# Performance work log

Measured on AMD Instinct MI355X. Metric: run time of the kernel, lower is better.

Reference implementation:

```python
import jax, jax.numpy as jnp
import numpy as np

N, M, D = 20000, 16000, 128

def setup_inputs() -> dict:
    key = jax.random.key(0)
    ks = jax.random.split(key, 4)
    return {
        "clear_feature": jax.random.normal(ks[0], (N, D), dtype=jnp.float32),
        "rain_feature": jax.random.normal(ks[1], (M, D), dtype=jnp.float32),
        # torch nn.Linear weight layout: (out_features, in_features)
        "W1": jax.random.normal(ks[2], (D, 2 * D), dtype=jnp.float32) * 0.05,
        "b1": jnp.zeros((D,), dtype=jnp.float32),
        "W2": jax.random.normal(ks[3], (1, D), dtype=jnp.float32) * 0.05,
        "b2": jnp.zeros((1,), dtype=jnp.float32),
    }

def reference(clear_feature, rain_feature, W1, b1, W2, b2):
    # --- KNN alignment (k=1): argmin of squared Euclidean distance == cdist+topk(smallest) ---
    x2 = jnp.sum(clear_feature * clear_feature, axis=-1, keepdims=True)   # [N,1]
    y2 = jnp.sum(rain_feature * rain_feature, axis=-1)                    # [M]
    d2 = x2 + y2 - 2.0 * (clear_feature @ rain_feature.T)                 # [N,M]
    idx = jnp.argmin(d2, axis=-1)                                         # [N]
    aligned = rain_feature[idx]                                           # [N,D] gather
    # --- attention MLP: Linear(2D->D) + ReLU + Linear(D->1) + Sigmoid ---
    comb = jnp.concatenate([clear_feature, aligned], axis=-1)             # [N,2D]
    h = jax.nn.relu(comb @ W1.T + b1)                                     # [N,D]
    w = jax.nn.sigmoid(h @ W2.T + b2)                                     # [N,1]
    # --- gated fusion ---
    return w * clear_feature + (1.0 - w) * aligned
```

## Files before the change

kernel.cpp:

```cpp
#include <hip/hip_runtime.h>
#include <stdint.h>

#define NN 20000
#define MM 16000
#define DD 128
#define NTILES_M 125
#define SPLITS 8
#define NBLK 157

typedef unsigned long long u64;
typedef _Float16 f16x8 __attribute__((ext_vector_type(8)));
typedef float f32x16 __attribute__((ext_vector_type(16)));

__global__ void k_init_keys(u64* keys) {
    int i = blockIdx.x * 256 + threadIdx.x;
    if (i < NN) keys[i] = ~0ull;
}

__global__ void k_y2(const float* __restrict__ rain, float* __restrict__ y2) {
    int row = blockIdx.x * 4 + (threadIdx.x >> 6);
    int lane = threadIdx.x & 63;
    if (row >= MM) return;
    float2 v = ((const float2*)(rain + (size_t)row * DD))[lane];
    float s = v.x * v.x + v.y * v.y;
    #pragma unroll
    for (int off = 32; off > 0; off >>= 1) s += __shfl_down(s, off);
    if (lane == 0) y2[row] = s;
}

__global__ void k_split_A(const float* __restrict__ clear_f,
                          _Float16* __restrict__ Ahi, _Float16* __restrict__ Alo) {
    int id = blockIdx.x * 256 + threadIdx.x;
    if (id >= NN * 16) return;
    int row = id >> 4, kc = id & 15;
    const float4* src = (const float4*)(clear_f + (size_t)row * DD + kc * 8);
    float4 v0 = src[0], v1 = src[1];
    float x[8] = {v0.x, v0.y, v0.z, v0.w, v1.x, v1.y, v1.z, v1.w};
    _Float16 hi[8], lo[8];
    #pragma unroll
    for (int j = 0; j < 8; ++j) {
        float s = -2.f * x[j];
        _Float16 h = (_Float16)s;
        hi[j] = h;
        lo[j] = (_Float16)(s - (float)h);
    }
    *(f16x8*)(Ahi + (size_t)row * DD + (size_t)kc * 8) = *(f16x8*)hi;
    *(f16x8*)(Alo + (size_t)row * DD + (size_t)kc * 8) = *(f16x8*)lo;
}

__global__ void k_split_B(const float* __restrict__ rain, _Float16* __restrict__ Bimg) {
    int id = blockIdx.x * 256 + threadIdx.x;
    if (id >= MM * 16) return;
    int row = id >> 4, kp = id & 15;
    int tile = row >> 7, c = row & 127;
    int cg = c >> 5, cc = c & 31;
    int kstep = kp >> 1, kh = kp & 1;
    int chunk = ((kstep * 4 + cg) * 2 + kh) * 32 + cc;
    const float4* src = (const float4*)(rain + (size_t)row * DD + kp * 8);
    float4 v0 = src[0], v1 = src[1];
    float x[8] = {v0.x, v0.y, v0.z, v0.w, v1.x, v1.y, v1.z, v1.w};
    _Float16 hi[8], lo[8];
    #pragma unroll
    for (int j = 0; j < 8; ++j) {
        _Float16 h = (_Float16)x[j];
        hi[j] = h;
        lo[j] = (_Float16)(x[j] - (float)h);
    }
    size_t tbase = (size_t)tile * 32768;
    *(f16x8*)(Bimg + tbase + (size_t)chunk * 8) = *(f16x8*)hi;
    *(f16x8*)(Bimg + tbase + 16384 + (size_t)chunk * 8) = *(f16x8*)lo;
}

__global__ __launch_bounds__(256, 2) void k_dist(
        const _Float16* __restrict__ Ahi, const _Float16* __restrict__ Alo,
        const _Float16* __restrict__ Bimg, const float* __restrict__ y2,
        u64* __restrict__ keys) {
    __shared__ _Float16 lds[32768];

    const int tid = threadIdx.x;
    const int w = tid >> 6, lane = tid & 63;
    const int l5 = lane >> 5, l31 = lane & 31;
    const int id = blockIdx.x;
    const int split = id & 7;
    const int n0 = (id >> 3) * 128;

    int arow = n0 + w * 32 + l31;
    if (arow >= NN) arow = NN - 1;
    const _Float16* ap = Ahi + (size_t)arow * DD + l5 * 8;
    const _Float16* lp = Alo + (size_t)arow * DD + l5 * 8;
    f16x8 afh[8], afl[8];
    #pragma unroll
    for (int ks = 0; ks < 8; ++ks) {
        afh[ks] = *(const f16x8*)(ap + ks * 16);
        afl[ks] = *(const f16x8*)(lp + ks * 16);
    }

    float bestd[16];
    int bestcol[16];
    #pragma unroll
    for (int r = 0; r < 16; ++r) { bestd[r] = 1e30f; bestcol[r] = 0; }

    for (int t = split; t < NTILES_M; t += SPLITS) {
        float y2v[4];
        #pragma unroll
        for (int cg = 0; cg < 4; ++cg) y2v[cg] = y2[t * 128 + cg * 32 + l31];

        {
            const _Float16* gsrc = Bimg + (size_t)t * 32768;
            #pragma unroll
            for (int n = 0; n < 16; ++n) {
                int seg = w * 16 + n;
                const _Float16* gp = gsrc + (size_t)seg * 512 + (size_t)lane * 8;
                _Float16* dst = lds + (size_t)seg * 512;
                __builtin_amdgcn_global_load_lds(
                    (const __attribute__((address_space(1))) unsigned int*)gp,
                    (__attribute__((address_space(3))) unsigned int*)dst,
                    16, 0, 0);
            }
        }
        __syncthreads();

        f32x16 acc[4];
        #pragma unroll
        for (int cg = 0; cg < 4; ++cg)
            #pragma unroll
            for (int e = 0; e < 16; ++e) acc[cg][e] = 0.f;

        #pragma unroll
        for (int ks = 0; ks < 8; ++ks) {
            f16x8 bh[4], bl[4];
            #pragma unroll
            for (int cg = 0; cg < 4; ++cg) {
                int chunk = (ks * 4 + cg) * 64 + lane;
                bh[cg] = *(const f16x8*)(lds + (size_t)chunk * 8);
                bl[cg] = *(const f16x8*)(lds + 16384 + (size_t)chunk * 8);
            }
            #pragma unroll
            for (int cg = 0; cg < 4; ++cg) {
                acc[cg] = __builtin_amdgcn_mfma_f32_32x32x16_f16(afh[ks], bh[cg], acc[cg], 0, 0, 0);
                acc[cg] = __builtin_amdgcn_mfma_f32_32x32x16_f16(afh[ks], bl[cg], acc[cg], 0, 0, 0);
                acc[cg] = __builtin_amdgcn_mfma_f32_32x32x16_f16(afl[ks], bh[cg], acc[cg], 0, 0, 0);
            }
        }

        int cb0 = t * 128 + l31;
        #pragma unroll
        for (int r = 0; r < 16; ++r) {
            float d0 = acc[0][r] + y2v[0];
            float d1 = acc[1][r] + y2v[1];
            float d2 = acc[2][r] + y2v[2];
            float d3 = acc[3][r] + y2v[3];
            float tmin = fminf(fminf(d0, d1), fminf(d2, d3));
            int nc = (d0 <= tmin) ? cb0
                   : (d1 <= tmin) ? cb0 + 32
                   : (d2 <= tmin) ? cb0 + 64 : cb0 + 96;
            bool upd = tmin < bestd[r];
            bestd[r] = upd ? tmin : bestd[r];
            bestcol[r] = upd ? nc : bestcol[r];
        }
        __syncthreads();
    }

    #pragma unroll
    for (int r = 0; r < 16; ++r) {
        unsigned u = __float_as_uint(bestd[r]);
        u ^= (unsigned)((int)u >> 31) | 0x80000000u;
        u64 key = ((u64)u << 32) | (unsigned)bestcol[r];
        #pragma unroll
        for (int off = 1; off < 32; off <<= 1) {
            u64 o = __shfl_xor(key, off);
            if (o < key) key = o;
        }
        if (l31 == 0) {
            int grow = n0 + w * 32 + (r & 3) + 8 * (r >> 2) + 4 * l5;
            if (grow < NN) atomicMin(&keys[grow], key);
        }
    }
}

__global__ __launch_bounds__(256) void k_mlp(const float* __restrict__ clear_f,
                                             const float* __restrict__ rain_f,
                                             const float* __restrict__ W1,
                                             const float* __restrict__ b1,
                                             const float* __restrict__ W2,
                                             const float* __restrict__ b2,
                                             const u64* __restrict__ keys,
                                             float* __restrict__ out) {
    __shared__ float comb_s[16][260];
    __shared__ float w1_s[64][132];
    __shared__ float red_s[16][17];
    __shared__ float w_s[16];

    const int tid = threadIdx.x;
    const int n0 = blockIdx.x * 16;

    {
        int r = tid >> 4;
        int t = tid & 15;
        int n = n0 + r;
        unsigned idx = (unsigned)(keys[n] & 0xffffffffu);
        const float4* cp = (const float4*)(clear_f + (size_t)n * DD);
        const float4* rp = (const float4*)(rain_f + (size_t)idx * DD);
        *(float4*)&comb_s[r][4 * t] = cp[t];
        *(float4*)&comb_s[r][4 * (t + 16)] = cp[t + 16];
        *(float4*)&comb_s[r][DD + 4 * t] = rp[t];
        *(float4*)&comb_s[r][DD + 4 * (t + 16)] = rp[t + 16];
    }

    const int r = tid & 15;
    const int g = tid >> 4;
    const int d8 = g * 8;
    float h[8] = {};
    for (int kt = 0; kt < 4; ++kt) {
        __syncthreads();
        #pragma unroll
        for (int i = 0; i < 32; ++i) {
            int lin = i * 256 + tid;
            int d = lin & 127;
            int kk = lin >> 7;
            w1_s[kk][d] = W1[(size_t)d * 256 + kt * 64 + kk];
        }
        __syncthreads();
        #pragma unroll
        for (int kk = 0; kk < 64; ++kk) {
            float c = comb_s[r][kt * 64 + kk];
            float4 wa = *(const float4*)&w1_s[kk][d8];
            float4 wb = *(const float4*)&w1_s[kk][d8 + 4];
            h[0] = fmaf(c, wa.x, h[0]);
            h[1] = fmaf(c, wa.y, h[1]);
            h[2] = fmaf(c, wa.z, h[2]);
            h[3] = fmaf(c, wa.w, h[3]);
            h[4] = fmaf(c, wb.x, h[4]);
            h[5] = fmaf(c, wb.y, h[5]);
            h[6] = fmaf(c, wb.z, h[6]);
            h[7] = fmaf(c, wb.w, h[7]);
        }
    }
    float part = 0.f;
    #pragma unroll
    for (int j = 0; j < 8; ++j) {
        float hv = h[j] + b1[d8 + j];
        hv = hv > 0.f ? hv : 0.f;
        part = fmaf(hv, W2[d8 + j], part);
    }
    red_s[r][g] = part;
    __syncthreads();
    if (tid < 16) {
        float s = 0.f;
        #pragma unroll
        for (int g2 = 0; g2 < 16; ++g2) s += red_s[tid][g2];
        s += b2[0];
        w_s[tid] = 1.f / (1.f + expf(-s));
    }
    __syncthreads();
    {
        int rw = tid >> 4;
        int c8 = (tid & 15) * 8;
        float wv = w_s[rw];
        float ov[8];
        #pragma unroll
        for (int j = 0; j < 8; ++j) {
            float cv = comb_s[rw][c8 + j];
            float av = comb_s[rw][DD + c8 + j];
            ov[j] = wv * cv + (1.f - wv) * av;
        }
        float4* o = (float4*)(out + (size_t)(n0 + rw) * DD + c8);
        o[0] = make_float4(ov[0], ov[1], ov[2], ov[3]);
        o[1] = make_float4(ov[4], ov[5], ov[6], ov[7]);
    }
}

extern "C" void kernel_launch(void* const* d_in, const int* in_sizes, int n_in,
                              void* d_out, int out_size, void* d_ws, size_t ws_size,
                              hipStream_t stream) {
    const float* clear_f = (const float*)d_in[0];
    const float* rain_f = (const float*)d_in[1];
    const float* W1 = (const float*)d_in[2];
    const float* b1 = (const float*)d_in[3];
    const float* W2 = (const float*)d_in[4];
    const float* b2 = (const float*)d_in[5];
    float* out = (float*)d_out;

    char* ws = (char*)d_ws;
    u64* keys = (u64*)ws;
    float* y2 = (float*)(ws + 160000);
    _Float16* Ahi = (_Float16*)(ws + 224000);
    _Float16* Alo = (_Float16*)(ws + 5344000);
    _Float16* Bimg = (_Float16*)(ws + 10464000);

    k_init_keys<<<(NN + 255) / 256, 256, 0, stream>>>(keys);
    k_y2<<<MM / 4, 256, 0, stream>>>(rain_f, y2);
    k_split_A<<<(NN * 16 + 255) / 256, 256, 0, stream>>>(clear_f, Ahi, Alo);
    k_split_B<<<(MM * 16 + 255) / 256, 256, 0, stream>>>(rain_f, Bimg);
    k_dist<<<NBLK * SPLITS, 256, 0, stream>>>(Ahi, Alo, Bimg, y2, keys);
    k_mlp<<<NN / 16, 256, 0, stream>>>(clear_f, rain_f, W1, b1, W2, b2, keys, out);
}
```

Baseline: 418.1 us.

## Retile distance kernel to 256x32 tiles with double-buffered LDS prefetch

The distance kernel now has each wave compute 64 A-rows against 32-column B tiles, so each block covers 256 rows. The next B tile is prefetched into a second LDS buffer while MFMAs run on the current one, and the grid is a 2D layout of 79 row blocks by 13 splits. The B image layout is simplified to match the 32-column tiles. The MLP kernel's W1 load is transposed so global reads are coalesced, with the LDS row padded to 133. Doubling the A fragments in registers raises register pressure and could lower occupancy.

```diff
diff --git a/kernel.cpp b/kernel.cpp
--- a/kernel.cpp
+++ b/kernel.cpp
@@ -4,9 +4,9 @@
 #define NN 20000
 #define MM 16000
 #define DD 128
-#define NTILES_M 125
-#define SPLITS 8
-#define NBLK 157
+#define CT 500
+#define SPLITS 13
+#define RB 79
 
 typedef unsigned long long u64;
 typedef _Float16 f16x8 __attribute__((ext_vector_type(8)));
@@ -51,11 +51,10 @@
 __global__ void k_split_B(const float* __restrict__ rain, _Float16* __restrict__ Bimg) {
     int id = blockIdx.x * 256 + threadIdx.x;
     if (id >= MM * 16) return;
-    int row = id >> 4, kp = id & 15;
-    int tile = row >> 7, c = row & 127;
-    int cg = c >> 5, cc = c & 31;
-    int kstep = kp >> 1, kh = kp & 1;
-    int chunk = ((kstep * 4 + cg) * 2 + kh) * 32 + cc;
+    int cl = id & 31;
+    int kp = (id >> 5) & 15;
+    int tc = id >> 9;
+    int row = tc * 32 + cl;
     const float4* src = (const float4*)(rain + (size_t)row * DD + kp * 8);
     float4 v0 = src[0], v1 = src[1];
     float x[8] = {v0.x, v0.y, v0.z, v0.w, v1.x, v1.y, v1.z, v1.w};
@@ -66,113 +65,131 @@
         hi[j] = h;
         lo[j] = (_Float16)(x[j] - (float)h);
     }
-    size_t tbase = (size_t)tile * 32768;
-    *(f16x8*)(Bimg + tbase + (size_t)chunk * 8) = *(f16x8*)hi;
-    *(f16x8*)(Bimg + tbase + 16384 + (size_t)chunk * 8) = *(f16x8*)lo;
+    size_t base = (size_t)tc * 8192;
+    int chunk = kp * 32 + cl;
+    *(f16x8*)(Bimg + base + (size_t)chunk * 8) = *(f16x8*)hi;
+    *(f16x8*)(Bimg + base + 4096 + (size_t)chunk * 8) = *(f16x8*)lo;
 }
 
 __global__ __launch_bounds__(256, 2) void k_dist(
         const _Float16* __restrict__ Ahi, const _Float16* __restrict__ Alo,
         const _Float16* __restrict__ Bimg, const float* __restrict__ y2,
         u64* __restrict__ keys) {
-    __shared__ _Float16 lds[32768];
+    __shared__ _Float16 lds[2][8192];
 
     const int tid = threadIdx.x;
     const int w = tid >> 6, lane = tid & 63;
     const int l5 = lane >> 5, l31 = lane & 31;
-    const int id = blockIdx.x;
-    const int split = id & 7;
-    const int n0 = (id >> 3) * 128;
-
-    int arow = n0 + w * 32 + l31;
-    if (arow >= NN) arow = NN - 1;
-    const _Float16* ap = Ahi + (size_t)arow * DD + l5 * 8;
-    const _Float16* lp = Alo + (size_t)arow * DD + l5 * 8;
-    f16x8 afh[8], afl[8];
-    #pragma unroll
-    for (int ks = 0; ks < 8; ++ks) {
-        afh[ks] = *(const f16x8*)(ap + ks * 16);
-        afl[ks] = *(const f16x8*)(lp + ks * 16);
-    }
-
-    float bestd[16];
-    int bestcol[16];
-    #pragma unroll
-    for (int r = 0; r < 16; ++r) { bestd[r] = 1e30f; bestcol[r] = 0; }
-
-    for (int t = split; t < NTILES_M; t += SPLITS) {
-        float y2v[4];
-        #pragma unroll
-        for (int cg = 0; cg < 4; ++cg) y2v[cg] = y2[t * 128 + cg * 32 + l31];
-
-        {
-            const _Float16* gsrc = Bimg + (size_t)t * 32768;
+    const int split = blockIdx.y;
+    const int n0 = blockIdx.x * 256;
+
+    f16x8 afh0[8], afl0[8], afh1[8], afl1[8];
+    {
+        int r0 = n0 + w * 64 + l31;       if (r0 >= NN) r0 = NN - 1;
+        int r1 = n0 + w * 64 + 32 + l31;  if (r1 >= NN) r1 = NN - 1;
+        const _Float16* h0 = Ahi + (size_t)r0 * DD + l5 * 8;
+        const _Float16* o0 = Alo + (size_t)r0 * DD + l5 * 8;
+        const _Float16* h1 = Ahi + (size_t)r1 * DD + l5 * 8;
+        const _Float16* o1 = Alo + (size_t)r1 * DD + l5 * 8;
+        #pragma unroll
+        for (int ks = 0; ks < 8; ++ks) {
+            afh0[ks] = *(const f16x8*)(h0 + ks * 16);
+            afl0[ks] = *(const f16x8*)(o0 + ks * 16);
+            afh1[ks] = *(const f16x8*)(h1 + ks * 16);
+            afl1[ks] = *(const f16x8*)(o1 + ks * 16);
+        }
+    }
+
+    float bestd[32];
+    int bestcol[32];
+    #pragma unroll
+    for (int s = 0; s < 32; ++s) { bestd[s] = 1e30f; bestcol[s] = 0; }
+
+    const int nt = (CT - split + SPLITS - 1) / SPLITS;
+
+    {
+        const _Float16* gsrc = Bimg + (size_t)split * 8192;
+        #pragma unroll
+        for (int n = 0; n < 4; ++n) {
+            int seg = w * 4 + n;
+            __builtin_amdgcn_global_load_lds(
+                (const __attribute__((address_space(1))) unsigned int*)
+                    (gsrc + (size_t)seg * 512 + (size_t)lane * 8),
+                (__attribute__((address_space(3))) unsigned int*)
+                    (&lds[0][0] + (size_t)seg * 512),
+                16, 0, 0);
+        }
+    }
+    __syncthreads();
+
+    int p = 0;
+    for (int i = 0; i < nt; ++i) {
+        const int t = split + i * SPLITS;
+
+        if (i + 1 < nt) {
+            const _Float16* gsrc = Bimg + (size_t)(t + SPLITS) * 8192;
+            _Float16* lbase = &lds[1 - p][0];
             #pragma unroll
-            for (int n = 0; n < 16; ++n) {
-                int seg = w * 16 + n;
-                const _Float16* gp = gsrc + (size_t)seg * 512 + (size_t)lane * 8;
-                _Float16* dst = lds + (size_t)seg * 512;
+            for (int n = 0; n < 4; ++n) {
+                int seg = w * 4 + n;
                 __builtin_amdgcn_global_load_lds(
-                    (const __attribute__((address_space(1))) unsigned int*)gp,
-                    (__attribute__((address_space(3))) unsigned int*)dst,
+                    (const __attribute__((address_space(1))) unsigned int*)
+                        (gsrc + (size_t)seg * 512 + (size_t)lane * 8),
+                    (__attribute__((address_space(3))) unsigned int*)
+                        (lbase + (size_t)seg * 512),
                     16, 0, 0);
             }
         }
+
+        float y2v = y2[t * 32 + l31];
+
+        f32x16 acc0, acc1;
+        #pragma unroll
+        for (int e = 0; e < 16; ++e) { acc0[e] = 0.f; acc1[e] = 0.f; }
+
+        const _Float16* lbuf = &lds[p][0];
+        #pragma unroll
+        for (int ks = 0; ks < 8; ++ks) {
+            f16x8 bh = *(const f16x8*)(lbuf + (size_t)ks * 512 + (size_t)lane * 8);
+            f16x8 bl = *(const f16x8*)(lbuf + 4096 + (size_t)ks * 512 + (size_t)lane * 8);
+            acc0 = __builtin_amdgcn_mfma_f32_32x32x16_f16(afh0[ks], bh, acc0, 0, 0, 0);
+            acc1 = __builtin_amdgcn_mfma_f32_32x32x16_f16(afh1[ks], bh, acc1, 0, 0, 0);
+            acc0 = __builtin_amdgcn_mfma_f32_32x32x16_f16(afh0[ks], bl, acc0, 0, 0, 0);
+            acc1 = __builtin_amdgcn_mfma_f32_32x32x16_f16(afh1[ks], bl, acc1, 0, 0, 0);
+            acc0 = __builtin_amdgcn_mfma_f32_32x32x16_f16(afl0[ks], bh, acc0, 0, 0, 0);
+            acc1 = __builtin_amdgcn_mfma_f32_32x32x16_f16(afl1[ks], bh, acc1, 0, 0, 0);
+        }
+
+        int col = t * 32 + l31;
+        #pragma unroll
+        for (int e = 0; e < 16; ++e) {
+            float d0 = acc0[e] + y2v;
+            bool u0 = d0 < bestd[e];
+            bestd[e] = u0 ? d0 : bestd[e];
+            bestcol[e] = u0 ? col : bestcol[e];
+            float d1 = acc1[e] + y2v;
+            bool u1 = d1 < bestd[16 + e];
+            bestd[16 + e] = u1 ? d1 : bestd[16 + e];
+            bestcol[16 + e] = u1 ? col : bestcol[16 + e];
+        }
+
         __syncthreads();
-
-        f32x16 acc[4];
-        #pragma unroll
-        for (int cg = 0; cg < 4; ++cg)
-            #pragma unroll
-            for (int e = 0; e < 16; ++e) acc[cg][e] = 0.f;
-
-        #pragma unroll
-        for (int ks = 0; ks < 8; ++ks) {
-            f16x8 bh[4], bl[4];
-            #pragma unroll
-            for (int cg = 0; cg < 4; ++cg) {
-                int chunk = (ks * 4 + cg) * 64 + lane;
-                bh[cg] = *(const f16x8*)(lds + (size_t)chunk * 8);
-                bl[cg] = *(const f16x8*)(lds + 16384 + (size_t)chunk * 8);
-            }
-            #pragma unroll
-            for (int cg = 0; cg < 4; ++cg) {
-                acc[cg] = __builtin_amdgcn_mfma_f32_32x32x16_f16(afh[ks], bh[cg], acc[cg], 0, 0, 0);
-                acc[cg] = __builtin_amdgcn_mfma_f32_32x32x16_f16(afh[ks], bl[cg], acc[cg], 0, 0, 0);
-                acc[cg] = __builtin_amdgcn_mfma_f32_32x32x16_f16(afl[ks], bh[cg], acc[cg], 0, 0, 0);
-            }
-        }
-
-        int cb0 = t * 128 + l31;
-        #pragma unroll
-        for (int r = 0; r < 16; ++r) {
-            float d0 = acc[0][r] + y2v[0];
-            float d1 = acc[1][r] + y2v[1];
-            float d2 = acc[2][r] + y2v[2];
-            float d3 = acc[3][r] + y2v[3];
-            float tmin = fminf(fminf(d0, d1), fminf(d2, d3));
-            int nc = (d0 <= tmin) ? cb0
-                   : (d1 <= tmin) ? cb0 + 32
-                   : (d2 <= tmin) ? cb0 + 64 : cb0 + 96;
-            bool upd = tmin < bestd[r];
-            bestd[r] = upd ? tmin : bestd[r];
-            bestcol[r] = upd ? nc : bestcol[r];
-        }
-        __syncthreads();
-    }
-
-    #pragma unroll
-    for (int r = 0; r < 16; ++r) {
-        unsigned u = __float_as_uint(bestd[r]);
-        u ^= (unsigned)((int)u >> 31) | 0x80000000u;
-        u64 key = ((u64)u << 32) | (unsigned)bestcol[r];
+        p ^= 1;
+    }
+
+    #pragma unroll
+    for (int s = 0; s < 32; ++s) {
+        unsigned u = __float_as_uint(bestd[s]);
+        u = (u & 0x80000000u) ? ~u : (u | 0x80000000u);
+        u64 key = ((u64)u << 32) | (unsigned)bestcol[s];
         #pragma unroll
         for (int off = 1; off < 32; off <<= 1) {
             u64 o = __shfl_xor(key, off);
             if (o < key) key = o;
         }
         if (l31 == 0) {
-            int grow = n0 + w * 32 + (r & 3) + 8 * (r >> 2) + 4 * l5;
+            int e = s & 15, rb = s >> 4;
+            int grow = n0 + w * 64 + rb * 32 + (e & 3) + 8 * (e >> 2) + 4 * l5;
             if (grow < NN) atomicMin(&keys[grow], key);
         }
     }
@@ -187,7 +204,7 @@
                                              const u64* __restrict__ keys,
                                              float* __restrict__ out) {
     __shared__ float comb_s[16][260];
-    __shared__ float w1_s[64][132];
+    __shared__ float w1_s[64][133];
     __shared__ float red_s[16][17];
     __shared__ float w_s[16];
 
@@ -216,8 +233,8 @@
         #pragma unroll
         for (int i = 0; i < 32; ++i) {
             int lin = i * 256 + tid;
-            int d = lin & 127;
-            int kk = lin >> 7;
+            int kk = lin & 63;
+            int d = lin >> 6;
             w1_s[kk][d] = W1[(size_t)d * 256 + kt * 64 + kk];
         }
         __syncthreads();
@@ -292,6 +309,6 @@
     k_y2<<<MM / 4, 256, 0, stream>>>(rain_f, y2);
     k_split_A<<<(NN * 16 + 255) / 256, 256, 0, stream>>>(clear_f, Ahi, Alo);
     k_split_B<<<(MM * 16 + 255) / 256, 256, 0, stream>>>(rain_f, Bimg);
-    k_dist<<<NBLK * SPLITS, 256, 0, stream>>>(Ahi, Alo, Bimg, y2, keys);
+    k_dist<<<dim3(RB, SPLITS), 256, 0, stream>>>(Ahi, Alo, Bimg, y2, keys);
     k_mlp<<<NN / 16, 256, 0, stream>>>(clear_f, rain_f, W1, b1, W2, b2, keys, out);
 }
```

New measurement: 393.5 us. -5.9%, faster.
